# Kernel optimization log

Measured on AMD Instinct MI355X. Metric: run time of the kernel, lower is better.

## Reference

```python
import jax, jax.numpy as jnp
import numpy as np

EPS = 1e-8
NUM_ITERATIONS = 3


def layer_norm(x, g, b, eps=EPS):
    m = jnp.mean(x, axis=-1, keepdims=True)
    v = jnp.mean((x - m) ** 2, axis=-1, keepdims=True)
    return (x - m) * jax.lax.rsqrt(v + eps) * g + b


def gru_cell(x, h, w_ih, w_hh, b_ih, b_hh):
    # PyTorch GRUCell: gates ordered (r, z, n)
    gi = x @ w_ih.T + b_ih  # [B*S, 3D]
    gh = h @ w_hh.T + b_hh
    i_r, i_z, i_n = jnp.split(gi, 3, axis=-1)
    h_r, h_z, h_n = jnp.split(gh, 3, axis=-1)
    r = jax.nn.sigmoid(i_r + h_r)
    z = jax.nn.sigmoid(i_z + h_z)
    n = jnp.tanh(i_n + r * h_n)
    return (1.0 - z) * n + z * h


def setup_inputs() -> dict:
    key = jax.random.key(0)
    ks = jax.random.split(key, 12)
    B, N, D, S = 64, 1024, 512, 16
    s = 1.0 / np.sqrt(D)
    return {
        "inputs": jax.random.normal(ks[0], (B, N, D), jnp.float32),
        "noise": jax.random.normal(ks[1], (B, S, D), jnp.float32),
        "slot_mu": jax.random.normal(ks[2], (1, 1, D), jnp.float32),
        "slot_log_sigma": jnp.zeros((1, 1, D), jnp.float32),
        "ln_in_g": jnp.ones((D,), jnp.float32),
        "ln_in_b": jnp.zeros((D,), jnp.float32),
        "ln_slots_g": jnp.ones((D,), jnp.float32),
        "ln_slots_b": jnp.zeros((D,), jnp.float32),
        "ln_mlp_g": jnp.ones((D,), jnp.float32),
        "ln_mlp_b": jnp.zeros((D,), jnp.float32),
        "Wq": jax.random.normal(ks[3], (D, D), jnp.float32) * s,
        "Wk": jax.random.normal(ks[4], (D, D), jnp.float32) * s,
        "Wv": jax.random.normal(ks[5], (D, D), jnp.float32) * s,
        "gru_w_ih": jax.random.normal(ks[6], (3 * D, D), jnp.float32) * s,
        "gru_w_hh": jax.random.normal(ks[7], (3 * D, D), jnp.float32) * s,
        "gru_b_ih": jnp.zeros((3 * D,), jnp.float32),
        "gru_b_hh": jnp.zeros((3 * D,), jnp.float32),
        "mlp_w1": jax.random.normal(ks[8], (D, D), jnp.float32) * s,
        "mlp_b1": jnp.zeros((D,), jnp.float32),
        "mlp_w2": jax.random.normal(ks[9], (D, D), jnp.float32) * s,
        "mlp_b2": jnp.zeros((D,), jnp.float32),
    }


def reference(inputs, noise, slot_mu, slot_log_sigma,
              ln_in_g, ln_in_b, ln_slots_g, ln_slots_b, ln_mlp_g, ln_mlp_b,
              Wq, Wk, Wv, gru_w_ih, gru_w_hh, gru_b_ih, gru_b_hh,
              mlp_w1, mlp_b1, mlp_w2, mlp_b2):
    B, N, D = inputs.shape
    S = noise.shape[1]
    scale = D ** (-0.5)

    # slot init: mu + sigma * eps
    slots = slot_mu + jnp.exp(slot_log_sigma) * noise  # [B,S,D]

    x = layer_norm(inputs, ln_in_g, ln_in_b)
    k = x @ Wk.T  # [B,N,D]
    v = x @ Wv.T

    for _ in range(NUM_ITERATIONS):
        slots_prev = slots
        sn = layer_norm(slots, ln_slots_g, ln_slots_b)
        q = sn @ Wq.T  # [B,S,D]
        attn_logits = jnp.einsum("bnd,bmd->bnm", q, k) * scale  # [B,S,N]
        attn = jax.nn.softmax(attn_logits, axis=-1)
        attn = attn / (jnp.sum(attn, axis=1, keepdims=True) + EPS)  # column-normalize over slots
        updates = jnp.einsum("bnm,bmd->bnd", attn, v)  # [B,S,D]
        slots = gru_cell(updates.reshape(-1, D), slots_prev.reshape(-1, D),
                         gru_w_ih, gru_w_hh, gru_b_ih, gru_b_hh).reshape(B, S, D)
        h = jax.nn.relu(layer_norm(slots, ln_mlp_g, ln_mlp_b) @ mlp_w1.T + mlp_b1)
        slots = slots + h @ mlp_w2.T + mlp_b2

    # proj_to_hidden is Identity (slot_dim == hidden_size); forward_dtype=float32
    return slots
```

## Files before the change

kernel.cpp:

```cpp
#include <hip/hip_runtime.h>
#include <hip/hip_bf16.h>
#include <cstdint>
#include <cstddef>


typedef __bf16 bf16x8 __attribute__((ext_vector_type(8)));
typedef float f32x4 __attribute__((ext_vector_type(4)));

__device__ __forceinline__ float bf2f(unsigned int u) {
  union { unsigned int i; float f; } v; v.i = u << 16; return v.f;
}
__device__ __forceinline__ unsigned short f2bf(float x) {
  __hip_bfloat16 h = __float2bfloat16(x);
  unsigned short u;
  __builtin_memcpy(&u, &h, 2);
  return u;
}

#define GLD16(gp, lp)                                                       \
  __builtin_amdgcn_global_load_lds(                                         \
      (const __attribute__((address_space(1))) void*)(gp),                  \
      (__attribute__((address_space(3))) void*)(lp), 16, 0, 0)


__global__ void wprep_k(const float* __restrict__ w1, const float* __restrict__ w2,
                        const float* __restrict__ wih, const float* __restrict__ whh,
                        const float* __restrict__ bih, const float* __restrict__ bhh,
                        const float* __restrict__ mu, const float* __restrict__ ls,
                        const float* __restrict__ noise,
                        unsigned short* __restrict__ w1_bf, unsigned short* __restrict__ w2_bf,
                        unsigned short* __restrict__ wih_bf, unsigned short* __restrict__ wcat,
                        float* __restrict__ bcat, float* __restrict__ slots) {
  int blk = blockIdx.x, t = threadIdx.x;
  if (blk < 1024) {
    int i = blk * 256 + t; w1_bf[i] = f2bf(w1[i]);
  } else if (blk < 2048) {
    int i = (blk - 1024) * 256 + t; w2_bf[i] = f2bf(w2[i]);
  } else if (blk < 5120) {
    int i = (blk - 2048) * 256 + t; wih_bf[i] = f2bf(wih[i]);
  } else if (blk < 7168) {
    int i = (blk - 5120) * 256 + t;
    int j = i >> 9, d = i & 511;
    wcat[(size_t)j * 1024 + 512 + d] = f2bf(whh[(size_t)j * 512 + d]);
  } else if (blk < 8192) {
    int i = (blk - 7168) * 256 + t;
    int j = i >> 9, d = i & 511;
    wcat[(size_t)(1536 + j) * 1024 + 512 + d] = f2bf(whh[(size_t)(1024 + j) * 512 + d]);
  } else if (blk < 10240) {
    int i = (blk - 8192) * 256 + t;
    if (i < 262144) {
      int j = i >> 9, d = i & 511;
      wcat[(size_t)(1536 + j) * 1024 + d] = 0;
    } else {
      int k = i - 262144;
      int j = k >> 9, d = k & 511;
      wcat[(size_t)(1024 + j) * 1024 + 512 + d] = 0;
    }
  } else if (blk < 10248) {
    int j = (blk - 10240) * 256 + t;
    float v;
    if (j < 1024)      v = bih[j] + bhh[j];
    else if (j < 1536) v = bih[j];
    else               v = bhh[j - 512];
    bcat[j] = v;
  } else {
    int i = (blk - 10248) * 256 + t;
    int d = i & 511;
    slots[i] = mu[d] + expf(ls[d]) * noise[i];
  }
}

__global__ __launch_bounds__(256) void tcast3_k(const float* __restrict__ Wq,
                                                const float* __restrict__ Wk,
                                                const float* __restrict__ Wv,
                                                unsigned short* __restrict__ wqT,
                                                unsigned short* __restrict__ wkT,
                                                unsigned short* __restrict__ wvT) {
  __shared__ float tt[32][33];
  const float* in = blockIdx.z == 0 ? Wq : (blockIdx.z == 1 ? Wk : Wv);
  unsigned short* out = blockIdx.z == 0 ? wqT : (blockIdx.z == 1 ? wkT : wvT);
  int c0 = blockIdx.x << 5, r0 = blockIdx.y << 5;
  int tx = threadIdx.x & 31, ty = threadIdx.x >> 5;
  #pragma unroll
  for (int i = 0; i < 4; ++i)
    tt[ty + 8 * i][tx] = in[(size_t)(r0 + ty + 8 * i) * 512 + c0 + tx];
  __syncthreads();
  #pragma unroll
  for (int i = 0; i < 4; ++i)
    out[(size_t)(c0 + ty + 8 * i) * 512 + r0 + tx] = f2bf(tt[tx][ty + 8 * i]);
}


__global__ __launch_bounds__(256) void ln_rows_k(
    const float* __restrict__ in, const float* __restrict__ g, const float* __restrict__ b,
    unsigned short* __restrict__ out, int rows) {
  int w = threadIdx.x >> 6, lane = threadIdx.x & 63;
  int row = (blockIdx.x << 2) + w;
  if (row >= rows) return;
  const float4* rp = reinterpret_cast<const float4*>(in + (size_t)row * 512);
  float4 v0 = rp[lane], v1 = rp[lane + 64];
  float s = v0.x + v0.y + v0.z + v0.w + v1.x + v1.y + v1.z + v1.w;
  float q = v0.x*v0.x + v0.y*v0.y + v0.z*v0.z + v0.w*v0.w
          + v1.x*v1.x + v1.y*v1.y + v1.z*v1.z + v1.w*v1.w;
  #pragma unroll
  for (int o = 32; o > 0; o >>= 1) { s += __shfl_xor(s, o); q += __shfl_xor(q, o); }
  float m = s * (1.0f / 512.0f);
  float rstd = rsqrtf(q * (1.0f / 512.0f) - m * m + 1e-8f);
  const float4* gp = reinterpret_cast<const float4*>(g);
  const float4* bp = reinterpret_cast<const float4*>(b);
  float4 g0 = gp[lane], g1 = gp[lane + 64];
  float4 b0 = bp[lane], b1 = bp[lane + 64];
  ushort4 o0, o1;
  o0.x = f2bf((v0.x - m) * rstd * g0.x + b0.x);
  o0.y = f2bf((v0.y - m) * rstd * g0.y + b0.y);
  o0.z = f2bf((v0.z - m) * rstd * g0.z + b0.z);
  o0.w = f2bf((v0.w - m) * rstd * g0.w + b0.w);
  o1.x = f2bf((v1.x - m) * rstd * g1.x + b1.x);
  o1.y = f2bf((v1.y - m) * rstd * g1.y + b1.y);
  o1.z = f2bf((v1.z - m) * rstd * g1.z + b1.z);
  o1.w = f2bf((v1.w - m) * rstd * g1.w + b1.w);
  ushort4* op = reinterpret_cast<ushort4*>(out + (size_t)row * 512);
  op[lane] = o0; op[lane + 64] = o1;
}


__global__ __launch_bounds__(256) void xt_k(const unsigned short* __restrict__ x,
                                            unsigned short* __restrict__ xT) {
  __shared__ unsigned short t[64][68];
  int nt = blockIdx.x, et = blockIdx.y, b = blockIdx.z;
  int r = threadIdx.x >> 3, c8 = (threadIdx.x & 7) << 3;
  #pragma unroll
  for (int p = 0; p < 2; ++p) {
    int row = r + (p << 5);
    *reinterpret_cast<uint4*>(&t[row][c8]) = *reinterpret_cast<const uint4*>(
        x + ((size_t)(b << 10) + (nt << 6) + row) * 512 + (et << 6) + c8);
  }
  __syncthreads();
  #pragma unroll
  for (int p = 0; p < 2; ++p) {
    int erow = r + (p << 5);
    ushort4 a, bb;
    #pragma unroll
    for (int j = 0; j < 4; ++j) ((unsigned short*)&a)[j] = t[c8 + j][erow];
    #pragma unroll
    for (int j = 0; j < 4; ++j) ((unsigned short*)&bb)[j] = t[c8 + 4 + j][erow];
    unsigned short* o = xT + ((size_t)(b << 9) + (et << 6) + erow) * 1024 + (nt << 6) + c8;
    *reinterpret_cast<ushort4*>(o) = a;
    *reinterpret_cast<ushort4*>(o + 4) = bb;
  }
}

__global__ __launch_bounds__(256) void gru_ln_k(
    const float* __restrict__ gates, const float* __restrict__ hp,
    const float* __restrict__ g, const float* __restrict__ b,
    float* __restrict__ sgru, unsigned short* __restrict__ lnm) {
  int w = threadIdx.x >> 6, lane = threadIdx.x & 63;
  int row = (blockIdx.x << 2) + w;
  size_t gb = (size_t)row * 2048 + (lane << 3);
  size_t hb = (size_t)row * 512 + (lane << 3);
  float rs[8], zs[8], in_[8], hn[8], hv[8], y[8];
  #pragma unroll
  for (int c = 0; c < 2; ++c) {
    *reinterpret_cast<float4*>(rs + 4*c)  = *reinterpret_cast<const float4*>(gates + gb + 4*c);
    *reinterpret_cast<float4*>(zs + 4*c)  = *reinterpret_cast<const float4*>(gates + gb + 512 + 4*c);
    *reinterpret_cast<float4*>(in_ + 4*c) = *reinterpret_cast<const float4*>(gates + gb + 1024 + 4*c);
    *reinterpret_cast<float4*>(hn + 4*c)  = *reinterpret_cast<const float4*>(gates + gb + 1536 + 4*c);
    *reinterpret_cast<float4*>(hv + 4*c)  = *reinterpret_cast<const float4*>(hp + hb + 4*c);
  }
  float s = 0.f, q = 0.f;
  #pragma unroll
  for (int j = 0; j < 8; ++j) {
    float r = 1.0f / (1.0f + expf(-rs[j]));
    float z = 1.0f / (1.0f + expf(-zs[j]));
    float n = tanhf(in_[j] + r * hn[j]);
    float h = (1.0f - z) * n + z * hv[j];
    y[j] = h; s += h; q += h * h;
  }
  #pragma unroll
  for (int o = 32; o > 0; o >>= 1) { s += __shfl_xor(s, o); q += __shfl_xor(q, o); }
  float m = s * (1.0f / 512.0f);
  float rstd = rsqrtf(q * (1.0f / 512.0f) - m * m + 1e-8f);
  const float* gg = g + (lane << 3);
  const float* bb = b + (lane << 3);
  #pragma unroll
  for (int c = 0; c < 2; ++c)
    *reinterpret_cast<float4*>(sgru + hb + 4*c) = *reinterpret_cast<const float4*>(y + 4*c);
  uint4 o4;
  unsigned int p[8];
  #pragma unroll
  for (int j = 0; j < 8; ++j) p[j] = f2bf((y[j] - m) * rstd * gg[j] + bb[j]);
  o4.x = p[0] | (p[1] << 16); o4.y = p[2] | (p[3] << 16);
  o4.z = p[4] | (p[5] << 16); o4.w = p[6] | (p[7] << 16);
  *reinterpret_cast<uint4*>(lnm + hb) = o4;
}


__global__ __launch_bounds__(256) void gemm_cat(
    const unsigned short* __restrict__ A, const unsigned short* __restrict__ W,
    unsigned short* __restrict__ Cout, int M, int N, int K, int ldc) {
  __shared__ unsigned short sA[2][8192];
  __shared__ unsigned short sB[2][8192];
  const int tid = threadIdx.x;
  const int lane = tid & 63, w = tid >> 6;

  int nwg = gridDim.x * gridDim.y;
  int flat = blockIdx.y * gridDim.x + blockIdx.x;
  if ((nwg & 7) == 0) { int c = nwg >> 3; flat = (flat & 7) * c + (flat >> 3); }
  const int row0 = (flat / gridDim.x) << 7;
  const int col0 = (flat % gridDim.x) << 7;

  const int wm = (w >> 1) << 6, wn = (w & 1) << 6;
  const int lrow = lane & 15, kt = (lane >> 4) << 3;
  const int sr8 = lane >> 3, sc8 = (lane & 7) << 3;

  f32x4 acc[4][4];
  #pragma unroll
  for (int m = 0; m < 4; ++m)
    #pragma unroll
    for (int n = 0; n < 4; ++n) acc[m][n] = f32x4{0.f, 0.f, 0.f, 0.f};

  auto stage = [&](int buf, int k0) {
    #pragma unroll
    for (int i = 0; i < 4; ++i) {
      int ii = (w << 2) + i;
      int r = (ii << 3) + sr8;
      GLD16(A + (size_t)(row0 + r) * K + k0 + sc8, &sA[buf][ii * 512]);
      GLD16(W + (size_t)(col0 + r) * K + k0 + sc8, &sB[buf][ii * 512]);
    }
  };

  stage(0, 0);
  const int nt = K >> 6;
  int cur = 0;
  for (int t = 0; t < nt; ++t) {
    __syncthreads();
    if (t + 1 < nt) stage(cur ^ 1, (t + 1) << 6);
    #pragma unroll
    for (int kk = 0; kk < 2; ++kk) {
      bf16x8 af[4], bfv[4];
      #pragma unroll
      for (int m = 0; m < 4; ++m)
        af[m] = *reinterpret_cast<const bf16x8*>(&sA[cur][(wm + m * 16 + lrow) * 64 + (kk << 5) + kt]);
      #pragma unroll
      for (int n = 0; n < 4; ++n)
        bfv[n] = *reinterpret_cast<const bf16x8*>(&sB[cur][(wn + n * 16 + lrow) * 64 + (kk << 5) + kt]);
      #pragma unroll
      for (int m = 0; m < 4; ++m)
        #pragma unroll
        for (int n = 0; n < 4; ++n)
          acc[m][n] = __builtin_amdgcn_mfma_f32_16x16x32_bf16(af[m], bfv[n], acc[m][n], 0, 0, 0);
    }
    cur ^= 1;
  }

  const int rb = (lane >> 4) << 2;
  #pragma unroll
  for (int m = 0; m < 4; ++m) {
    #pragma unroll
    for (int n = 0; n < 4; ++n) {
      int col = col0 + wn + n * 16 + lrow;
      #pragma unroll
      for (int r = 0; r < 4; ++r) {
        int row = row0 + wm + m * 16 + rb + r;
        Cout[(size_t)row * ldc + col] = f2bf(acc[m][n][r]);
      }
    }
  }
}


__global__ __launch_bounds__(256) void q2ln_k(
    const float* __restrict__ slots, const float* __restrict__ g, const float* __restrict__ b,
    const unsigned short* __restrict__ wpt, unsigned short* __restrict__ q2,
    unsigned short* __restrict__ A2) {
  __shared__ unsigned short s_sn[16 * 520];
  __shared__ unsigned short sB[2][8192];
  const int b_ = blockIdx.y, ct = blockIdx.x;
  const int lane = threadIdx.x & 63, w = threadIdx.x >> 6;
  const int lrow = lane & 15, kt = (lane >> 4) << 3;
  const int sr8 = lane >> 3, sc8 = (lane & 7) << 3;

  const float4* gp = reinterpret_cast<const float4*>(g);
  const float4* bp = reinterpret_cast<const float4*>(b);
  float4 g0 = gp[lane], g1 = gp[lane + 64];
  float4 b0 = bp[lane], b1 = bp[lane + 64];
  #pragma unroll
  for (int rr = 0; rr < 4; ++rr) {
    int r = w * 4 + rr;
    const float4* rp = reinterpret_cast<const float4*>(slots + (size_t)(b_ * 16 + r) * 512);
    float4 v0 = rp[lane], v1 = rp[lane + 64];
    float s = v0.x + v0.y + v0.z + v0.w + v1.x + v1.y + v1.z + v1.w;
    float q = v0.x*v0.x + v0.y*v0.y + v0.z*v0.z + v0.w*v0.w
            + v1.x*v1.x + v1.y*v1.y + v1.z*v1.z + v1.w*v1.w;
    #pragma unroll
    for (int o = 32; o > 0; o >>= 1) { s += __shfl_xor(s, o); q += __shfl_xor(q, o); }
    float m = s * (1.0f / 512.0f);
    float rstd = rsqrtf(q * (1.0f / 512.0f) - m * m + 1e-8f);
    ushort4 o0, o1;
    o0.x = f2bf((v0.x - m) * rstd * g0.x + b0.x);
    o0.y = f2bf((v0.y - m) * rstd * g0.y + b0.y);
    o0.z = f2bf((v0.z - m) * rstd * g0.z + b0.z);
    o0.w = f2bf((v0.w - m) * rstd * g0.w + b0.w);
    o1.x = f2bf((v1.x - m) * rstd * g1.x + b1.x);
    o1.y = f2bf((v1.y - m) * rstd * g1.y + b1.y);
    o1.z = f2bf((v1.z - m) * rstd * g1.z + b1.z);
    o1.w = f2bf((v1.w - m) * rstd * g1.w + b1.w);
    *reinterpret_cast<ushort4*>(&s_sn[r * 520 + lane * 4]) = o0;
    *reinterpret_cast<ushort4*>(&s_sn[r * 520 + 256 + lane * 4]) = o1;
    if (ct == 0) {
      ushort4 c0, c1;
      c0.x = f2bf(v0.x); c0.y = f2bf(v0.y); c0.z = f2bf(v0.z); c0.w = f2bf(v0.w);
      c1.x = f2bf(v1.x); c1.y = f2bf(v1.y); c1.z = f2bf(v1.z); c1.w = f2bf(v1.w);
      unsigned short* a2r = A2 + (size_t)(b_ * 16 + r) * 1024 + 512;
      *reinterpret_cast<ushort4*>(a2r + lane * 4) = c0;
      *reinterpret_cast<ushort4*>(a2r + 256 + lane * 4) = c1;
    }
  }

  const unsigned short* Bb = wpt + (size_t)(ct << 7) * 512;
  auto stage = [&](int buf, int k0) {
    #pragma unroll
    for (int i = 0; i < 4; ++i) {
      int ii = (w << 2) + i;
      GLD16(Bb + (size_t)((ii << 3) + sr8) * 512 + k0 + sc8, &sB[buf][ii * 512]);
    }
  };

  f32x4 acc[2];
  acc[0] = f32x4{0.f, 0.f, 0.f, 0.f};
  acc[1] = f32x4{0.f, 0.f, 0.f, 0.f};

  stage(0, 0);
  int cur = 0;
  for (int t = 0; t < 8; ++t) {
    __syncthreads();
    if (t + 1 < 8) stage(cur ^ 1, (t + 1) << 6);
    #pragma unroll
    for (int kk = 0; kk < 2; ++kk) {
      bf16x8 af = *reinterpret_cast<const bf16x8*>(&s_sn[lrow * 520 + (t << 6) + (kk << 5) + kt]);
      #pragma unroll
      for (int ni = 0; ni < 2; ++ni) {
        bf16x8 bfv = *reinterpret_cast<const bf16x8*>(
            &sB[cur][((w * 2 + ni) * 16 + lrow) * 64 + (kk << 5) + kt]);
        acc[ni] = __builtin_amdgcn_mfma_f32_16x16x32_bf16(af, bfv, acc[ni], 0, 0, 0);
      }
    }
    cur ^= 1;
  }

  const int rb = (lane >> 4) << 2;
  #pragma unroll
  for (int ni = 0; ni < 2; ++ni) {
    int col = (ct << 7) + (w * 2 + ni) * 16 + lrow;
    #pragma unroll
    for (int r = 0; r < 4; ++r) {
      int s = rb + r;
      q2[(size_t)((b_ << 4) + s) * 512 + col] = f2bf(acc[ni][r]);
    }
  }
}


__global__ __launch_bounds__(256) void logits_k(
    const unsigned short* __restrict__ q2, const unsigned short* __restrict__ x,
    unsigned short* __restrict__ out, float* __restrict__ lstats) {
  __shared__ unsigned short sA[2][1024];
  __shared__ unsigned short sB[2][8192];
  __shared__ float sstat[16][4][2];
  const int b = blockIdx.y, nt = blockIdx.x;
  const int lane = threadIdx.x & 63, w = threadIdx.x >> 6;
  const int lrow = lane & 15, kt = (lane >> 4) << 3;
  const int sr8 = lane >> 3, sc8 = (lane & 7) << 3;
  const unsigned short* Ab = q2 + ((size_t)b << 13);
  const unsigned short* Bb = x + (((size_t)(b << 10) + (nt << 7)) << 9);

  f32x4 acc[2];
  acc[0] = f32x4{0.f, 0.f, 0.f, 0.f};
  acc[1] = f32x4{0.f, 0.f, 0.f, 0.f};

  auto stage = [&](int buf, int k0) {
    #pragma unroll
    for (int i = 0; i < 4; ++i) {
      int ii = (w << 2) + i;
      GLD16(Bb + (size_t)((ii << 3) + sr8) * 512 + k0 + sc8, &sB[buf][ii * 512]);
    }
    if (w == 0) {
      #pragma unroll
      for (int i = 0; i < 2; ++i)
        GLD16(Ab + (size_t)((i << 3) + sr8) * 512 + k0 + sc8, &sA[buf][i * 512]);
    }
  };

  stage(0, 0);
  int cur = 0;
  for (int t = 0; t < 8; ++t) {
    __syncthreads();
    if (t + 1 < 8) stage(cur ^ 1, (t + 1) << 6);
    #pragma unroll
    for (int kk = 0; kk < 2; ++kk) {
      bf16x8 af = *reinterpret_cast<const bf16x8*>(&sA[cur][lrow * 64 + (kk << 5) + kt]);
      #pragma unroll
      for (int ni = 0; ni < 2; ++ni) {
        bf16x8 bfv = *reinterpret_cast<const bf16x8*>(
            &sB[cur][((w * 2 + ni) * 16 + lrow) * 64 + (kk << 5) + kt]);
        acc[ni] = __builtin_amdgcn_mfma_f32_16x16x32_bf16(af, bfv, acc[ni], 0, 0, 0);
      }
    }
    cur ^= 1;
  }

  const int rb = (lane >> 4) << 2;
  unsigned short lv[2][4];
  #pragma unroll
  for (int ni = 0; ni < 2; ++ni) {
    int n = (nt << 7) + (w * 2 + ni) * 16 + lrow;
    #pragma unroll
    for (int r = 0; r < 4; ++r) {
      unsigned short u = f2bf(acc[ni][r]);
      lv[ni][r] = u;
      out[(size_t)((b << 4) + rb + r) * 1024 + n] = u;
    }
  }
  #pragma unroll
  for (int r = 0; r < 4; ++r) {
    float v0 = bf2f(lv[0][r]), v1 = bf2f(lv[1][r]);
    float m = fmaxf(v0, v1);
    #pragma unroll
    for (int o = 1; o < 16; o <<= 1) m = fmaxf(m, __shfl_xor(m, o));
    float l = __expf(v0 - m) + __expf(v1 - m);
    #pragma unroll
    for (int o = 1; o < 16; o <<= 1) l += __shfl_xor(l, o);
    if (lrow == 0) { sstat[rb + r][w][0] = m; sstat[rb + r][w][1] = l; }
  }
  __syncthreads();
  if (threadIdx.x < 16) {
    int s = threadIdx.x;
    float m = sstat[s][0][0];
    #pragma unroll
    for (int c = 1; c < 4; ++c) m = fmaxf(m, sstat[s][c][0]);
    float l = 0.f;
    #pragma unroll
    for (int c = 0; c < 4; ++c) l += sstat[s][c][1] * __expf(sstat[s][c][0] - m);
    float* lp = lstats + (((size_t)(b << 4) + s) * 8 + nt) * 2;
    lp[0] = m; lp[1] = l;
  }
}


__global__ __launch_bounds__(256) void pv_sm_k(
    const unsigned short* __restrict__ logits, const float* __restrict__ lstats,
    const unsigned short* __restrict__ xT, unsigned short* __restrict__ A2) {
  __shared__ float s_mi[16][2];
  __shared__ unsigned short s_at[16 * 1032];
  __shared__ unsigned short sA[2][8192];
  const int b_ = blockIdx.y, et = blockIdx.x;
  const int lane = threadIdx.x & 63, w = threadIdx.x >> 6;
  const int lrow = lane & 15, kt = (lane >> 4) << 3;
  const int sr8 = lane >> 3, sc8 = (lane & 7) << 3;
  const unsigned short* lg = logits + ((size_t)b_ << 14);

  if (threadIdx.x < 16) {
    int s = threadIdx.x;
    const float* lp = lstats + (((size_t)(b_ << 4) + s) * 8) * 2;
    float m = lp[0];
    #pragma unroll
    for (int c = 1; c < 8; ++c) m = fmaxf(m, lp[c * 2]);
    float l = 0.f;
    #pragma unroll
    for (int c = 0; c < 8; ++c) l += lp[c * 2 + 1] * __expf(lp[c * 2] - m);
    s_mi[s][0] = m; s_mi[s][1] = 1.0f / l;
  }
  __syncthreads();

  #pragma unroll
  for (int j = 0; j < 4; ++j) {
    int c = threadIdx.x + (j << 8);
    float e[16];
    float cs = 0.f;
    #pragma unroll
    for (int s = 0; s < 16; ++s) {
      e[s] = __expf(bf2f(lg[(size_t)s * 1024 + c]) - s_mi[s][0]) * s_mi[s][1];
      cs += e[s];
    }
    float rv = 1.0f / (cs + 1e-8f);
    #pragma unroll
    for (int s = 0; s < 16; ++s) s_at[s * 1032 + c] = f2bf(e[s] * rv);
  }

  const unsigned short* Ab = xT + ((size_t)b_ << 19) + (size_t)(et << 7) * 1024;
  auto stage = [&](int buf, int k0) {
    #pragma unroll
    for (int i = 0; i < 4; ++i) {
      int ii = (w << 2) + i;
      GLD16(Ab + (size_t)((ii << 3) + sr8) * 1024 + k0 + sc8, &sA[buf][ii * 512]);
    }
  };

  f32x4 acc[2];
  acc[0] = f32x4{0.f, 0.f, 0.f, 0.f};
  acc[1] = f32x4{0.f, 0.f, 0.f, 0.f};

  stage(0, 0);
  int cur = 0;
  for (int t = 0; t < 16; ++t) {
    __syncthreads();
    if (t + 1 < 16) stage(cur ^ 1, (t + 1) << 6);
    #pragma unroll
    for (int kk = 0; kk < 2; ++kk) {
      bf16x8 bfv = *reinterpret_cast<const bf16x8*>(&s_at[lrow * 1032 + (t << 6) + (kk << 5) + kt]);
      #pragma unroll
      for (int mi = 0; mi < 2; ++mi) {
        bf16x8 af = *reinterpret_cast<const bf16x8*>(
            &sA[cur][((w * 2 + mi) * 16 + lrow) * 64 + (kk << 5) + kt]);
        acc[mi] = __builtin_amdgcn_mfma_f32_16x16x32_bf16(af, bfv, acc[mi], 0, 0, 0);
      }
    }
    cur ^= 1;
  }

  const int rb = (lane >> 4) << 2;
  const int s = lrow;
  #pragma unroll
  for (int mi = 0; mi < 2; ++mi) {
    int e0 = (et << 7) + (w * 2 + mi) * 16 + rb;
    ushort4 o;
    o.x = f2bf(acc[mi][0]); o.y = f2bf(acc[mi][1]);
    o.z = f2bf(acc[mi][2]); o.w = f2bf(acc[mi][3]);
    *reinterpret_cast<ushort4*>(&A2[(size_t)((b_ << 4) + s) * 1024 + e0]) = o;
  }
}


template<int BIAS, int RELU, int ADDSRC, int OUTBF16, int SCALE>
__global__ __launch_bounds__(256) void gemm_sm(
    const unsigned short* __restrict__ A, const unsigned short* __restrict__ W,
    const float* __restrict__ bias, const float* __restrict__ addsrc,
    void* __restrict__ Cout, int M, int N, int K, float scalev) {
  __shared__ unsigned short sA[2][4096];
  __shared__ unsigned short sB[2][4096];
  const int tid = threadIdx.x;
  const int lane = tid & 63, w = tid >> 6;

  int nwg = gridDim.x * gridDim.y;
  int flat = blockIdx.y * gridDim.x + blockIdx.x;
  if ((nwg & 7) == 0) { int c = nwg >> 3; flat = (flat & 7) * c + (flat >> 3); }
  const int row0 = (flat / gridDim.x) << 6;
  const int col0 = (flat % gridDim.x) << 6;

  const int lrow = lane & 15, kt = (lane >> 4) << 3;
  const int sr8 = lane >> 3, sc8 = (lane & 7) << 3;

  f32x4 acc[4];
  #pragma unroll
  for (int m = 0; m < 4; ++m) acc[m] = f32x4{0.f, 0.f, 0.f, 0.f};

  auto stage = [&](int buf, int k0) {
    #pragma unroll
    for (int i = 0; i < 2; ++i) {
      int ii = (w << 1) + i;
      int r = (ii << 3) + sr8;
      GLD16(A + (size_t)(row0 + r) * K + k0 + sc8, &sA[buf][ii * 512]);
      GLD16(W + (size_t)(col0 + r) * K + k0 + sc8, &sB[buf][ii * 512]);
    }
  };

  stage(0, 0);
  const int nt = K >> 6;
  int cur = 0;
  for (int t = 0; t < nt; ++t) {
    __syncthreads();
    if (t + 1 < nt) stage(cur ^ 1, (t + 1) << 6);
    #pragma unroll
    for (int kk = 0; kk < 2; ++kk) {
      bf16x8 bfv = *reinterpret_cast<const bf16x8*>(
          &sB[cur][((w << 4) + lrow) * 64 + (kk << 5) + kt]);
      #pragma unroll
      for (int m = 0; m < 4; ++m) {
        bf16x8 af = *reinterpret_cast<const bf16x8*>(
            &sA[cur][(m * 16 + lrow) * 64 + (kk << 5) + kt]);
        acc[m] = __builtin_amdgcn_mfma_f32_16x16x32_bf16(af, bfv, acc[m], 0, 0, 0);
      }
    }
    cur ^= 1;
  }

  const int rb = (lane >> 4) << 2;
  const int col = col0 + (w << 4) + lrow;
  float bv = BIAS ? bias[col] : 0.0f;
  #pragma unroll
  for (int m = 0; m < 4; ++m) {
    #pragma unroll
    for (int r = 0; r < 4; ++r) {
      int row = row0 + m * 16 + rb + r;
      float v = acc[m][r];
      if (SCALE) v *= scalev;
      v += bv;
      if (ADDSRC) v += addsrc[(size_t)row * N + col];
      if (RELU) v = fmaxf(v, 0.0f);
      if (OUTBF16) ((unsigned short*)Cout)[(size_t)row * N + col] = f2bf(v);
      else ((float*)Cout)[(size_t)row * N + col] = v;
    }
  }
}


extern "C" void kernel_launch(void* const* d_in, const int* in_sizes, int n_in,
                              void* d_out, int out_size, void* d_ws, size_t ws_size,
                              hipStream_t stream) {
  const float* inputs  = (const float*)d_in[0];
  const float* noise   = (const float*)d_in[1];
  const float* slot_mu = (const float*)d_in[2];
  const float* slot_ls = (const float*)d_in[3];
  const float* ln_in_g = (const float*)d_in[4];
  const float* ln_in_b = (const float*)d_in[5];
  const float* ln_s_g  = (const float*)d_in[6];
  const float* ln_s_b  = (const float*)d_in[7];
  const float* ln_m_g  = (const float*)d_in[8];
  const float* ln_m_b  = (const float*)d_in[9];
  const float* Wq   = (const float*)d_in[10];
  const float* Wk   = (const float*)d_in[11];
  const float* Wv   = (const float*)d_in[12];
  const float* w_ih = (const float*)d_in[13];
  const float* w_hh = (const float*)d_in[14];
  const float* b_ih = (const float*)d_in[15];
  const float* b_hh = (const float*)d_in[16];
  const float* w1   = (const float*)d_in[17];
  const float* b1   = (const float*)d_in[18];
  const float* w2   = (const float*)d_in[19];
  const float* b2   = (const float*)d_in[20];

  const int BN = 65536, BS = 1024;

  uintptr_t base = (uintptr_t)d_ws;
  auto alloc = [&](size_t bytes) {
    void* p = (void*)base;
    base += (bytes + 255) & ~(size_t)255;
    return p;
  };
  unsigned short* x_bf    = (unsigned short*)alloc((size_t)BN * 512 * 2);
  unsigned short* xT      = (unsigned short*)alloc((size_t)64 * 512 * 1024 * 2);
  unsigned short* wqT     = (unsigned short*)alloc(512 * 512 * 2);
  unsigned short* wkT     = (unsigned short*)alloc(512 * 512 * 2);
  unsigned short* wvT     = (unsigned short*)alloc(512 * 512 * 2);
  unsigned short* wpt     = (unsigned short*)alloc(512 * 512 * 2);
  unsigned short* wih_bf  = (unsigned short*)alloc((size_t)1536 * 512 * 2);
  unsigned short* wcat_bf = (unsigned short*)alloc((size_t)2048 * 1024 * 2);
  float*          bcat    = (float*)alloc(2048 * 4);
  unsigned short* w1_bf   = (unsigned short*)alloc(512 * 512 * 2);
  unsigned short* w2_bf   = (unsigned short*)alloc(512 * 512 * 2);
  float*          slots   = (float*)alloc((size_t)BS * 512 * 4);
  unsigned short* A2      = (unsigned short*)alloc((size_t)BS * 1024 * 2);
  unsigned short* q2_bf   = (unsigned short*)alloc((size_t)BS * 512 * 2);
  unsigned short* logits  = (unsigned short*)alloc((size_t)64 * 16 * 1024 * 2);
  float*          lstats  = (float*)alloc((size_t)64 * 16 * 8 * 2 * 4);
  float*          gates   = (float*)alloc((size_t)BS * 2048 * 4);
  float*          sgru    = (float*)alloc((size_t)BS * 512 * 4);
  unsigned short* lnm_bf  = (unsigned short*)alloc((size_t)BS * 512 * 2);
  unsigned short* h_bf    = (unsigned short*)alloc((size_t)BS * 512 * 2);
  (void)ws_size; (void)n_in; (void)in_sizes; (void)out_size;

  const float scale = 0.044194173824159216f;

  wprep_k<<<12296, 256, 0, stream>>>(w1, w2, w_ih, w_hh, b_ih, b_hh,
                                     slot_mu, slot_ls, noise,
                                     w1_bf, w2_bf, wih_bf, wcat_bf, bcat, slots);
  tcast3_k<<<dim3(16, 16, 3), 256, 0, stream>>>(Wq, Wk, Wv, wqT, wkT, wvT);
  gemm_sm<0,0,0,1,1><<<dim3(8, 8), 256, 0, stream>>>(
      wkT, wqT, nullptr, nullptr, wpt, 512, 512, 512, scale);
  gemm_cat<<<dim3(4, 12), 256, 0, stream>>>(
      wih_bf, wvT, wcat_bf, 1536, 512, 512, 1024);
  ln_rows_k<<<16384, 256, 0, stream>>>(inputs, ln_in_g, ln_in_b, x_bf, BN);
  xt_k<<<dim3(16, 8, 64), 256, 0, stream>>>(x_bf, xT);

  for (int it = 0; it < 3; ++it) {
    q2ln_k<<<dim3(4, 64), 256, 0, stream>>>(slots, ln_s_g, ln_s_b, wpt, q2_bf, A2);
    logits_k<<<dim3(8, 64), 256, 0, stream>>>(q2_bf, x_bf, logits, lstats);
    pv_sm_k<<<dim3(4, 64), 256, 0, stream>>>(logits, lstats, xT, A2);
    gemm_sm<1,0,0,0,0><<<dim3(32, 16), 256, 0, stream>>>(
        A2, wcat_bf, bcat, nullptr, gates, BS, 2048, 1024, 1.0f);
    gru_ln_k<<<256, 256, 0, stream>>>(gates, slots, ln_m_g, ln_m_b, sgru, lnm_bf);
    gemm_sm<1,1,0,1,0><<<dim3(8, 16), 256, 0, stream>>>(
        lnm_bf, w1_bf, b1, nullptr, h_bf, BS, 512, 512, 1.0f);
    float* slots_out = (it == 2) ? (float*)d_out : slots;
    gemm_sm<1,0,1,0,0><<<dim3(8, 16), 256, 0, stream>>>(
        h_bf, w2_bf, b2, sgru, slots_out, BS, 512, 512, 1.0f);
  }
}
```

Baseline: 322.5 us.

## Fuse prep kernels, merge LN with transpose, skip zero K-blocks in gates GEMM

The Wq/Wk/Wv transpose-cast moves into the weight-prep kernel, and the two precompute GEMMs (Wk^T·Wq and W_ih·Wv) are merged into one launch. Input layernorm and the x transpose become one kernel that stages normalized rows in shared memory, so the bf16 x is not re-read from global memory. The gates GEMM now skips the half of K that is structurally zero for the n-gate column blocks. Together these cut launch count, global traffic and wasted MFMA work, at the cost of more shared memory in the merged kernels and uneven work across gate column tiles.

```diff
diff --git a/kernel.cpp b/kernel.cpp
--- a/kernel.cpp
+++ b/kernel.cpp
@@ -28,9 +28,14 @@
                         const float* __restrict__ bih, const float* __restrict__ bhh,
                         const float* __restrict__ mu, const float* __restrict__ ls,
                         const float* __restrict__ noise,
+                        const float* __restrict__ Wq, const float* __restrict__ Wk,
+                        const float* __restrict__ Wv,
                         unsigned short* __restrict__ w1_bf, unsigned short* __restrict__ w2_bf,
                         unsigned short* __restrict__ wih_bf, unsigned short* __restrict__ wcat,
-                        float* __restrict__ bcat, float* __restrict__ slots) {
+                        float* __restrict__ bcat, float* __restrict__ slots,
+                        unsigned short* __restrict__ wqT, unsigned short* __restrict__ wkT,
+                        unsigned short* __restrict__ wvT) {
+  __shared__ float tt[32][33];
   int blk = blockIdx.x, t = threadIdx.x;
   if (blk < 1024) {
     int i = blk * 256 + t; w1_bf[i] = f2bf(w1[i]);
@@ -63,90 +68,84 @@
     else if (j < 1536) v = bih[j];
     else               v = bhh[j - 512];
     bcat[j] = v;
-  } else {
+  } else if (blk < 12296) {
     int i = (blk - 10248) * 256 + t;
     int d = i & 511;
     slots[i] = mu[d] + expf(ls[d]) * noise[i];
-  }
-}
-
-__global__ __launch_bounds__(256) void tcast3_k(const float* __restrict__ Wq,
-                                                const float* __restrict__ Wk,
-                                                const float* __restrict__ Wv,
-                                                unsigned short* __restrict__ wqT,
-                                                unsigned short* __restrict__ wkT,
-                                                unsigned short* __restrict__ wvT) {
-  __shared__ float tt[32][33];
-  const float* in = blockIdx.z == 0 ? Wq : (blockIdx.z == 1 ? Wk : Wv);
-  unsigned short* out = blockIdx.z == 0 ? wqT : (blockIdx.z == 1 ? wkT : wvT);
-  int c0 = blockIdx.x << 5, r0 = blockIdx.y << 5;
-  int tx = threadIdx.x & 31, ty = threadIdx.x >> 5;
-  #pragma unroll
-  for (int i = 0; i < 4; ++i)
-    tt[ty + 8 * i][tx] = in[(size_t)(r0 + ty + 8 * i) * 512 + c0 + tx];
-  __syncthreads();
-  #pragma unroll
-  for (int i = 0; i < 4; ++i)
-    out[(size_t)(c0 + ty + 8 * i) * 512 + r0 + tx] = f2bf(tt[tx][ty + 8 * i]);
-}
-
-
-__global__ __launch_bounds__(256) void ln_rows_k(
+  } else {
+    int blk2 = blk - 12296;
+    int mat = blk2 >> 8, tile = blk2 & 255;
+    const float* in = mat == 0 ? Wq : (mat == 1 ? Wk : Wv);
+    unsigned short* out = mat == 0 ? wqT : (mat == 1 ? wkT : wvT);
+    int c0 = (tile & 15) << 5, r0 = (tile >> 4) << 5;
+    int tx = t & 31, ty = t >> 5;
+    #pragma unroll
+    for (int i = 0; i < 4; ++i)
+      tt[ty + 8 * i][tx] = in[(size_t)(r0 + ty + 8 * i) * 512 + c0 + tx];
+    __syncthreads();
+    #pragma unroll
+    for (int i = 0; i < 4; ++i)
+      out[(size_t)(c0 + ty + 8 * i) * 512 + r0 + tx] = f2bf(tt[tx][ty + 8 * i]);
+  }
+}
+
+
+__global__ __launch_bounds__(256) void ln_xt_k(
     const float* __restrict__ in, const float* __restrict__ g, const float* __restrict__ b,
-    unsigned short* __restrict__ out, int rows) {
-  int w = threadIdx.x >> 6, lane = threadIdx.x & 63;
-  int row = (blockIdx.x << 2) + w;
-  if (row >= rows) return;
-  const float4* rp = reinterpret_cast<const float4*>(in + (size_t)row * 512);
-  float4 v0 = rp[lane], v1 = rp[lane + 64];
-  float s = v0.x + v0.y + v0.z + v0.w + v1.x + v1.y + v1.z + v1.w;
-  float q = v0.x*v0.x + v0.y*v0.y + v0.z*v0.z + v0.w*v0.w
-          + v1.x*v1.x + v1.y*v1.y + v1.z*v1.z + v1.w*v1.w;
-  #pragma unroll
-  for (int o = 32; o > 0; o >>= 1) { s += __shfl_xor(s, o); q += __shfl_xor(q, o); }
-  float m = s * (1.0f / 512.0f);
-  float rstd = rsqrtf(q * (1.0f / 512.0f) - m * m + 1e-8f);
+    unsigned short* __restrict__ x_bf, unsigned short* __restrict__ xT) {
+  __shared__ unsigned short tbuf[32 * 520];
+  const int row0 = blockIdx.x << 5;
+  const int bb_ = row0 >> 10;
+  const int n0 = row0 & 1023;
+  const int w = threadIdx.x >> 6, lane = threadIdx.x & 63;
+
   const float4* gp = reinterpret_cast<const float4*>(g);
   const float4* bp = reinterpret_cast<const float4*>(b);
   float4 g0 = gp[lane], g1 = gp[lane + 64];
   float4 b0 = bp[lane], b1 = bp[lane + 64];
-  ushort4 o0, o1;
-  o0.x = f2bf((v0.x - m) * rstd * g0.x + b0.x);
-  o0.y = f2bf((v0.y - m) * rstd * g0.y + b0.y);
-  o0.z = f2bf((v0.z - m) * rstd * g0.z + b0.z);
-  o0.w = f2bf((v0.w - m) * rstd * g0.w + b0.w);
-  o1.x = f2bf((v1.x - m) * rstd * g1.x + b1.x);
-  o1.y = f2bf((v1.y - m) * rstd * g1.y + b1.y);
-  o1.z = f2bf((v1.z - m) * rstd * g1.z + b1.z);
-  o1.w = f2bf((v1.w - m) * rstd * g1.w + b1.w);
-  ushort4* op = reinterpret_cast<ushort4*>(out + (size_t)row * 512);
-  op[lane] = o0; op[lane + 64] = o1;
-}
-
-
-__global__ __launch_bounds__(256) void xt_k(const unsigned short* __restrict__ x,
-                                            unsigned short* __restrict__ xT) {
-  __shared__ unsigned short t[64][68];
-  int nt = blockIdx.x, et = blockIdx.y, b = blockIdx.z;
-  int r = threadIdx.x >> 3, c8 = (threadIdx.x & 7) << 3;
-  #pragma unroll
-  for (int p = 0; p < 2; ++p) {
-    int row = r + (p << 5);
-    *reinterpret_cast<uint4*>(&t[row][c8]) = *reinterpret_cast<const uint4*>(
-        x + ((size_t)(b << 10) + (nt << 6) + row) * 512 + (et << 6) + c8);
+
+  #pragma unroll
+  for (int i = 0; i < 8; ++i) {
+    int r = (w << 3) + i;
+    int row = row0 + r;
+    const float4* rp = reinterpret_cast<const float4*>(in + (size_t)row * 512);
+    float4 v0 = rp[lane], v1 = rp[lane + 64];
+    float s = v0.x + v0.y + v0.z + v0.w + v1.x + v1.y + v1.z + v1.w;
+    float q = v0.x*v0.x + v0.y*v0.y + v0.z*v0.z + v0.w*v0.w
+            + v1.x*v1.x + v1.y*v1.y + v1.z*v1.z + v1.w*v1.w;
+    #pragma unroll
+    for (int o = 32; o > 0; o >>= 1) { s += __shfl_xor(s, o); q += __shfl_xor(q, o); }
+    float m = s * (1.0f / 512.0f);
+    float rstd = rsqrtf(q * (1.0f / 512.0f) - m * m + 1e-8f);
+    ushort4 o0, o1;
+    o0.x = f2bf((v0.x - m) * rstd * g0.x + b0.x);
+    o0.y = f2bf((v0.y - m) * rstd * g0.y + b0.y);
+    o0.z = f2bf((v0.z - m) * rstd * g0.z + b0.z);
+    o0.w = f2bf((v0.w - m) * rstd * g0.w + b0.w);
+    o1.x = f2bf((v1.x - m) * rstd * g1.x + b1.x);
+    o1.y = f2bf((v1.y - m) * rstd * g1.y + b1.y);
+    o1.z = f2bf((v1.z - m) * rstd * g1.z + b1.z);
+    o1.w = f2bf((v1.w - m) * rstd * g1.w + b1.w);
+    ushort4* op = reinterpret_cast<ushort4*>(x_bf + (size_t)row * 512);
+    op[lane] = o0; op[lane + 64] = o1;
+    *reinterpret_cast<ushort4*>(&tbuf[r * 520 + lane * 4]) = o0;
+    *reinterpret_cast<ushort4*>(&tbuf[r * 520 + 256 + lane * 4]) = o1;
   }
   __syncthreads();
-  #pragma unroll
-  for (int p = 0; p < 2; ++p) {
-    int erow = r + (p << 5);
-    ushort4 a, bb;
-    #pragma unroll
-    for (int j = 0; j < 4; ++j) ((unsigned short*)&a)[j] = t[c8 + j][erow];
-    #pragma unroll
-    for (int j = 0; j < 4; ++j) ((unsigned short*)&bb)[j] = t[c8 + 4 + j][erow];
-    unsigned short* o = xT + ((size_t)(b << 9) + (et << 6) + erow) * 1024 + (nt << 6) + c8;
+
+  const int e_lo = threadIdx.x >> 2;
+  const int n8 = (threadIdx.x & 3) << 3;
+  #pragma unroll
+  for (int et = 0; et < 8; ++et) {
+    int e = (et << 6) + e_lo;
+    ushort4 a, c;
+    #pragma unroll
+    for (int j = 0; j < 4; ++j) ((unsigned short*)&a)[j] = tbuf[(n8 + j) * 520 + e];
+    #pragma unroll
+    for (int j = 0; j < 4; ++j) ((unsigned short*)&c)[j] = tbuf[(n8 + 4 + j) * 520 + e];
+    unsigned short* o = xT + ((size_t)(bb_ << 9) + e) * 1024 + n0 + n8;
     *reinterpret_cast<ushort4*>(o) = a;
-    *reinterpret_cast<ushort4*>(o + 4) = bb;
+    *reinterpret_cast<ushort4*>(o + 4) = c;
   }
 }
 
@@ -195,19 +194,28 @@
 }
 
 
-__global__ __launch_bounds__(256) void gemm_cat(
-    const unsigned short* __restrict__ A, const unsigned short* __restrict__ W,
-    unsigned short* __restrict__ Cout, int M, int N, int K, int ldc) {
+__global__ __launch_bounds__(256) void gemm_pre(
+    const unsigned short* __restrict__ wih_bf, const unsigned short* __restrict__ wvT,
+    const unsigned short* __restrict__ wkT, const unsigned short* __restrict__ wqT,
+    unsigned short* __restrict__ wcat, unsigned short* __restrict__ wpt, float scale) {
   __shared__ unsigned short sA[2][8192];
   __shared__ unsigned short sB[2][8192];
-  const int tid = threadIdx.x;
-  const int lane = tid & 63, w = tid >> 6;
-
-  int nwg = gridDim.x * gridDim.y;
-  int flat = blockIdx.y * gridDim.x + blockIdx.x;
-  if ((nwg & 7) == 0) { int c = nwg >> 3; flat = (flat & 7) * c + (flat >> 3); }
-  const int row0 = (flat / gridDim.x) << 7;
-  const int col0 = (flat % gridDim.x) << 7;
+  const int blk = blockIdx.x;
+  const int lane = threadIdx.x & 63, w = threadIdx.x >> 6;
+
+  const unsigned short *A, *W;
+  unsigned short* C;
+  int row0, col0, ldc;
+  float sc;
+  if (blk < 48) {
+    A = wih_bf; W = wvT; C = wcat; ldc = 1024; sc = 1.0f;
+    row0 = (blk >> 2) << 7; col0 = (blk & 3) << 7;
+  } else {
+    A = wkT; W = wqT; C = wpt; ldc = 512; sc = scale;
+    int f = blk - 48;
+    row0 = (f >> 2) << 7; col0 = (f & 3) << 7;
+  }
+  const int K = 512;
 
   const int wm = (w >> 1) << 6, wn = (w & 1) << 6;
   const int lrow = lane & 15, kt = (lane >> 4) << 3;
@@ -230,11 +238,10 @@
   };
 
   stage(0, 0);
-  const int nt = K >> 6;
   int cur = 0;
-  for (int t = 0; t < nt; ++t) {
+  for (int t = 0; t < 8; ++t) {
     __syncthreads();
-    if (t + 1 < nt) stage(cur ^ 1, (t + 1) << 6);
+    if (t + 1 < 8) stage(cur ^ 1, (t + 1) << 6);
     #pragma unroll
     for (int kk = 0; kk < 2; ++kk) {
       bf16x8 af[4], bfv[4];
@@ -262,7 +269,7 @@
       #pragma unroll
       for (int r = 0; r < 4; ++r) {
         int row = row0 + wm + m * 16 + rb + r;
-        Cout[(size_t)row * ldc + col] = f2bf(acc[m][n][r]);
+        C[(size_t)row * ldc + col] = f2bf(acc[m][n][r] * sc);
       }
     }
   }
@@ -531,11 +538,11 @@
 }
 
 
-template<int BIAS, int RELU, int ADDSRC, int OUTBF16, int SCALE>
+template<int BIAS, int RELU, int ADDSRC, int OUTBF16, int GATES>
 __global__ __launch_bounds__(256) void gemm_sm(
     const unsigned short* __restrict__ A, const unsigned short* __restrict__ W,
     const float* __restrict__ bias, const float* __restrict__ addsrc,
-    void* __restrict__ Cout, int M, int N, int K, float scalev) {
+    void* __restrict__ Cout, int M, int N, int K) {
   __shared__ unsigned short sA[2][4096];
   __shared__ unsigned short sB[2][4096];
   const int tid = threadIdx.x;
@@ -547,6 +554,12 @@
   const int row0 = (flat / gridDim.x) << 6;
   const int col0 = (flat % gridDim.x) << 6;
 
+  int kb = 0, ke = K;
+  if (GATES) {
+    if (col0 >= 1536)      { kb = 512; ke = 1024; }
+    else if (col0 >= 1024) { kb = 0;   ke = 512;  }
+  }
+
   const int lrow = lane & 15, kt = (lane >> 4) << 3;
   const int sr8 = lane >> 3, sc8 = (lane & 7) << 3;
 
@@ -564,12 +577,12 @@
     }
   };
 
-  stage(0, 0);
-  const int nt = K >> 6;
+  stage(0, kb);
+  const int nt = (ke - kb) >> 6;
   int cur = 0;
   for (int t = 0; t < nt; ++t) {
     __syncthreads();
-    if (t + 1 < nt) stage(cur ^ 1, (t + 1) << 6);
+    if (t + 1 < nt) stage(cur ^ 1, kb + ((t + 1) << 6));
     #pragma unroll
     for (int kk = 0; kk < 2; ++kk) {
       bf16x8 bfv = *reinterpret_cast<const bf16x8*>(
@@ -592,9 +605,7 @@
     #pragma unroll
     for (int r = 0; r < 4; ++r) {
       int row = row0 + m * 16 + rb + r;
-      float v = acc[m][r];
-      if (SCALE) v *= scalev;
-      v += bv;
+      float v = acc[m][r] + bv;
       if (ADDSRC) v += addsrc[(size_t)row * N + col];
       if (RELU) v = fmaxf(v, 0.0f);
       if (OUTBF16) ((unsigned short*)Cout)[(size_t)row * N + col] = f2bf(v);
@@ -661,28 +672,24 @@
 
   const float scale = 0.044194173824159216f;
 
-  wprep_k<<<12296, 256, 0, stream>>>(w1, w2, w_ih, w_hh, b_ih, b_hh,
-                                     slot_mu, slot_ls, noise,
-                                     w1_bf, w2_bf, wih_bf, wcat_bf, bcat, slots);
-  tcast3_k<<<dim3(16, 16, 3), 256, 0, stream>>>(Wq, Wk, Wv, wqT, wkT, wvT);
-  gemm_sm<0,0,0,1,1><<<dim3(8, 8), 256, 0, stream>>>(
-      wkT, wqT, nullptr, nullptr, wpt, 512, 512, 512, scale);
-  gemm_cat<<<dim3(4, 12), 256, 0, stream>>>(
-      wih_bf, wvT, wcat_bf, 1536, 512, 512, 1024);
-  ln_rows_k<<<16384, 256, 0, stream>>>(inputs, ln_in_g, ln_in_b, x_bf, BN);
-  xt_k<<<dim3(16, 8, 64), 256, 0, stream>>>(x_bf, xT);
+  wprep_k<<<13064, 256, 0, stream>>>(w1, w2, w_ih, w_hh, b_ih, b_hh,
+                                     slot_mu, slot_ls, noise, Wq, Wk, Wv,
+                                     w1_bf, w2_bf, wih_bf, wcat_bf, bcat, slots,
+                                     wqT, wkT, wvT);
+  gemm_pre<<<64, 256, 0, stream>>>(wih_bf, wvT, wkT, wqT, wcat_bf, wpt, scale);
+  ln_xt_k<<<2048, 256, 0, stream>>>(inputs, ln_in_g, ln_in_b, x_bf, xT);
 
   for (int it = 0; it < 3; ++it) {
     q2ln_k<<<dim3(4, 64), 256, 0, stream>>>(slots, ln_s_g, ln_s_b, wpt, q2_bf, A2);
     logits_k<<<dim3(8, 64), 256, 0, stream>>>(q2_bf, x_bf, logits, lstats);
     pv_sm_k<<<dim3(4, 64), 256, 0, stream>>>(logits, lstats, xT, A2);
-    gemm_sm<1,0,0,0,0><<<dim3(32, 16), 256, 0, stream>>>(
-        A2, wcat_bf, bcat, nullptr, gates, BS, 2048, 1024, 1.0f);
+    gemm_sm<1,0,0,0,1><<<dim3(32, 16), 256, 0, stream>>>(
+        A2, wcat_bf, bcat, nullptr, gates, BS, 2048, 1024);
     gru_ln_k<<<256, 256, 0, stream>>>(gates, slots, ln_m_g, ln_m_b, sgru, lnm_bf);
     gemm_sm<1,1,0,1,0><<<dim3(8, 16), 256, 0, stream>>>(
-        lnm_bf, w1_bf, b1, nullptr, h_bf, BS, 512, 512, 1.0f);
+        lnm_bf, w1_bf, b1, nullptr, h_bf, BS, 512, 512);
     float* slots_out = (it == 2) ? (float*)d_out : slots;
     gemm_sm<1,0,1,0,0><<<dim3(8, 16), 256, 0, stream>>>(
-        h_bf, w2_bf, b2, sgru, slots_out, BS, 512, 512, 1.0f);
-  }
-}
+        h_bf, w2_bf, b2, sgru, slots_out, BS, 512, 512);
+  }
+}
```

After: 311.0 us. 3.5% less time.
